# Optimization experiments

Hardware: AMD Instinct MI355X
Metric: run time of the kernel (lower is better)

## Reference

```python
import jax, jax.numpy as jnp
import numpy as np

B, S, D = 2, 2048, 2048
QH, KVH, HD = 32, 8, 64
GRP = QH // KVH  # GQA group size = 4


def setup_inputs() -> dict:
    key = jax.random.key(0)
    ks = jax.random.split(key, 9)
    x = jax.random.normal(ks[0], (B, S, D), jnp.float32)
    # RoPE angle table: [S, HD//2] -> stacked (cos, sin) -> [S, HD//2, 2]
    inv_freq = 1.0 / (10000.0 ** (np.arange(0, HD, 2, dtype=np.float32) / HD))
    ang = np.arange(S, dtype=np.float32)[:, None] * inv_freq[None, :]
    freqs = jnp.stack([jnp.cos(jnp.asarray(ang)), jnp.sin(jnp.asarray(ang))], axis=-1).astype(jnp.float32)
    w = 0.02
    Wq = jax.random.normal(ks[1], (D, QH * HD), jnp.float32) * w
    bq = jnp.zeros((QH * HD,), jnp.float32)
    Wk = jax.random.normal(ks[2], (D, KVH * HD), jnp.float32) * w
    bk = jnp.zeros((KVH * HD,), jnp.float32)
    Wv = jax.random.normal(ks[3], (D, KVH * HD), jnp.float32) * w
    bv = jnp.zeros((KVH * HD,), jnp.float32)
    Wo = jax.random.normal(ks[4], (QH * HD, D), jnp.float32) * w
    bo = jnp.zeros((D,), jnp.float32)
    return {"x": x, "freqs": freqs, "Wq": Wq, "bq": bq, "Wk": Wk, "bk": bk,
            "Wv": Wv, "bv": bv, "Wo": Wo, "bo": bo}


def _rope(xh, cos, sin):
    # xh: [b, s, h, hd]; complex rotation on adjacent pairs, like view_as_complex
    b, s, h, hd = xh.shape
    xp = xh.reshape(b, s, h, hd // 2, 2)
    x0, x1 = xp[..., 0], xp[..., 1]
    o0 = x0 * cos - x1 * sin
    o1 = x0 * sin + x1 * cos
    return jnp.stack([o0, o1], axis=-1).reshape(b, s, h, hd)


def reference(x, freqs, Wq, bq, Wk, bk, Wv, bv, Wo, bo):
    b, s, _ = x.shape
    q = (x @ Wq + bq).reshape(b, s, QH, HD)
    k = (x @ Wk + bk).reshape(b, s, KVH, HD)
    v = (x @ Wv + bv).reshape(b, s, KVH, HD)
    cos = freqs[:s, :, 0][None, :, None, :]  # [1, s, 1, hd//2]
    sin = freqs[:s, :, 1][None, :, None, :]
    q = _rope(q, cos, sin)
    k = _rope(k, cos, sin)
    # [b, h, s, hd]
    q = q.transpose(0, 2, 1, 3).reshape(b, KVH, GRP, s, HD)
    k = k.transpose(0, 2, 1, 3)  # [b, kvh, s, hd]
    v = v.transpose(0, 2, 1, 3)
    scores = jnp.einsum('bkgsh,bkth->bkgst', q, k) / jnp.sqrt(jnp.float32(HD))
    attn = jax.nn.softmax(scores, axis=-1)
    o = jnp.einsum('bkgst,bkth->bkgsh', attn, v)  # [b, kvh, grp, s, hd]
    o = o.reshape(b, QH, s, HD).transpose(0, 2, 1, 3).reshape(b, s, QH * HD)
    return o @ Wo + bo
```

## Files before the change

### kernel.cpp

```cpp
#include <hip/hip_runtime.h>
#include <stdint.h>

#define B_   2
#define S_   2048
#define D_   2048
#define QH_  32
#define KVH_ 8
#define HD_  64

typedef short  short8  __attribute__((ext_vector_type(8)));
typedef float  floatx4 __attribute__((ext_vector_type(4)));

__device__ __forceinline__ ushort f2b(float f) {
  union { float f; uint32_t u; } c; c.f = f;
  uint32_t u = c.u;
  return (ushort)((u + 0x7FFFu + ((u >> 16) & 1u)) >> 16);
}

__device__ __forceinline__ uint32_t fbits(float f) {
  union { float f; uint32_t u; } c; c.f = f;
  return c.u;
}

__device__ __forceinline__ short8 mk8(uint32_t a, uint32_t b, uint32_t c, uint32_t d) {
  union { uint4 u; short8 s; } v; v.u = (uint4){a, b, c, d}; return v.s;
}

__device__ __forceinline__ uint32_t cvtpk(float a, float b) {
  uint32_t r;
  asm("v_cvt_pk_bf16_f32 %0, %1, %2" : "=v"(r) : "v"(a), "v"(b));
  return r;
}

__device__ __forceinline__ void dma16(const void* g, void* l) {
  __builtin_amdgcn_global_load_lds(
      (const __attribute__((address_space(1))) uint32_t*)(uintptr_t)g,
      (__attribute__((address_space(3))) uint32_t*)(uintptr_t)l, 16, 0, 0);
}

#define QSCALE 0.18033688f


__global__ __launch_bounds__(256) void conv_x_kernel(const float* __restrict__ X,
                                                     ushort* __restrict__ Xb) {
  size_t i = ((size_t)blockIdx.x * 256 + threadIdx.x) * 4;
  float4 v = *(const float4*)(X + i);
  ushort4 o;
  o.x = f2b(v.x); o.y = f2b(v.y); o.z = f2b(v.z); o.w = f2b(v.w);
  *(ushort4*)(Xb + i) = o;
}

__global__ void tconv_all_kernel(const float* __restrict__ Wq, const float* __restrict__ Wk,
                                 const float* __restrict__ Wv, const float* __restrict__ Wo,
                                 ushort* __restrict__ wqkv, ushort* __restrict__ wo) {
  __shared__ float tile[32][33];
  int z = blockIdx.z;
  const float* W; ushort* Wt; int N;
  if (z == 0)      { W = Wq; Wt = wqkv;                        N = 2048; }
  else if (z == 1) { W = Wk; Wt = wqkv + (size_t)2048 * 2048;  N = 512;  }
  else if (z == 2) { W = Wv; Wt = wqkv + (size_t)2560 * 2048;  N = 512;  }
  else             { W = Wo; Wt = wo;                          N = 2048; }
  int bx = blockIdx.x, by = blockIdx.y;
  if (bx * 32 >= N) return;
  int tx = threadIdx.x, ty = threadIdx.y;
#pragma unroll
  for (int i = 0; i < 32; i += 8)
    tile[ty + i][tx] = W[(size_t)(by * 32 + ty + i) * N + bx * 32 + tx];
  __syncthreads();
#pragma unroll
  for (int i = 0; i < 32; i += 8)
    Wt[(size_t)(bx * 32 + ty + i) * 2048 + by * 32 + tx] = f2b(tile[tx][ty + i]);
}

__global__ void bias_kernel(const float* __restrict__ bq, const float* __restrict__ bk,
                            const float* __restrict__ bv, float* __restrict__ outb) {
  int i = blockIdx.x * 256 + threadIdx.x;
  if (i >= 3072) return;
  float v;
  if (i < 2048)      v = bq[i];
  else if (i < 2560) v = bk[i - 2048];
  else               v = bv[i - 2560];
  outb[i] = v;
}


__global__ __launch_bounds__(256) void gemm_qkv_kernel(
    const ushort* __restrict__ A, const ushort* __restrict__ Bt,
    const float* __restrict__ bias, const float2* __restrict__ F2,
    ushort* __restrict__ qb, ushort* __restrict__ kb, ushort* __restrict__ vb) {
  const int K = 2048;
  __shared__ ushort sA[2][128 * 32];
  __shared__ ushort sB[2][128 * 32];
  const int tid  = threadIdx.x;
  const int bm   = blockIdx.y, bn = blockIdx.x;
  const int wave = tid >> 6, lane = tid & 63;
  const int quad = lane >> 4, l16 = lane & 15;
  const int wm   = (wave >> 1) * 64, wn = (wave & 1) * 64;

  const ushort* Ab = A  + (size_t)(bm * 128) * K;
  const ushort* Bb = Bt + (size_t)(bn * 128) * K;

  const int gr = lane >> 2;
  const int gu = (lane & 3) * 8;

  floatx4 acc[4][4];
#pragma unroll
  for (int i = 0; i < 4; i++)
#pragma unroll
    for (int j = 0; j < 4; j++) acc[i][j] = (floatx4){0.f, 0.f, 0.f, 0.f};

#pragma unroll
  for (int j = 0; j < 2; j++) {
    int row = j * 64 + wave * 16 + gr;
    dma16(Ab + (size_t)row * K + gu, &sA[0][j * 2048 + wave * 512]);
    dma16(Bb + (size_t)row * K + gu, &sB[0][j * 2048 + wave * 512]);
  }

  int cur = 0;
  for (int k0 = 0; k0 < K; k0 += 32) {
    __syncthreads();
    if (k0 + 32 < K) {
      int nxt = cur ^ 1;
#pragma unroll
      for (int j = 0; j < 2; j++) {
        int row = j * 64 + wave * 16 + gr;
        dma16(Ab + (size_t)row * K + k0 + 32 + gu, &sA[nxt][j * 2048 + wave * 512]);
        dma16(Bb + (size_t)row * K + k0 + 32 + gu, &sB[nxt][j * 2048 + wave * 512]);
      }
    }
    short8 af[4], bf[4];
#pragma unroll
    for (int mi = 0; mi < 4; mi++)
      af[mi] = *(const short8*)&sA[cur][(wm + mi * 16 + l16) * 32 + quad * 8];
#pragma unroll
    for (int ni = 0; ni < 4; ni++)
      bf[ni] = *(const short8*)&sB[cur][(wn + ni * 16 + l16) * 32 + quad * 8];
#pragma unroll
    for (int mi = 0; mi < 4; mi++)
#pragma unroll
      for (int ni = 0; ni < 4; ni++)
        acc[mi][ni] = __builtin_amdgcn_mfma_f32_16x16x32_bf16(
            af[mi], bf[ni], acc[mi][ni], 0, 0, 0);
    cur ^= 1;
  }

  const int isQ = (bn < 16);
  const int isV = (bn >= 20);
  const int hh  = wn >> 6;
  const float sySign = (l16 & 1) ? 1.f : -1.f;
  ushort* dst;
  int hbase;
  if (isQ)      { dst = qb; hbase = bn * 2 + hh; }
  else if (!isV){ dst = kb; hbase = (bn - 16) * 2 + hh; }
  else          { dst = vb; hbase = (bn - 20) * 2 + hh; }
  const int NH = isQ ? QH_ : KVH_;

  float bvv[4];
#pragma unroll
  for (int ni = 0; ni < 4; ni++)
    bvv[ni] = bias[bn * 128 + wn + ni * 16 + l16];

#pragma unroll
  for (int mi = 0; mi < 4; mi++) {
#pragma unroll
    for (int r = 0; r < 4; r++) {
      int row = bm * 128 + wm + mi * 16 + quad * 4 + r;
      int s = row & 2047, bb = row >> 11;
      size_t base = (((size_t)bb * NH + hbase) * S_ + s) * HD_ + l16 * 4;
      ushort4 pk;
      if (!isV) {
        float o[4];
#pragma unroll
        for (int ni = 0; ni < 4; ni++) {
          float xv = acc[mi][ni][r] + bvv[ni];
          float2 cs = F2[s * 32 + ni * 8 + (l16 >> 1)];
          float pp = __shfl_xor(xv, 1);
          float oo = fmaf(pp * sySign, cs.y, xv * cs.x);
          if (isQ) oo *= QSCALE;
          o[ni] = oo;
        }
        pk.x = f2b(o[0]); pk.y = f2b(o[1]); pk.z = f2b(o[2]); pk.w = f2b(o[3]);
      } else {
        pk.x = f2b(acc[mi][0][r] + bvv[0]);
        pk.y = f2b(acc[mi][1][r] + bvv[1]);
        pk.z = f2b(acc[mi][2][r] + bvv[2]);
        pk.w = f2b(acc[mi][3][r] + bvv[3]);
      }
      *(ushort4*)&dst[base] = pk;
    }
  }
}


__global__ __launch_bounds__(256) void gemm_bt_kernel(
    const ushort* __restrict__ A, const ushort* __restrict__ Bt,
    const float* __restrict__ bias, float* __restrict__ C,
    int M, int N, int K) {
  __shared__ ushort sA[2][128 * 32];
  __shared__ ushort sB[2][128 * 32];
  const int tid  = threadIdx.x;
  const int bm   = blockIdx.y, bn = blockIdx.x;
  const int wave = tid >> 6, lane = tid & 63;
  const int quad = lane >> 4, l16 = lane & 15;
  const int wm   = (wave >> 1) * 64, wn = (wave & 1) * 64;

  const ushort* Ab = A  + (size_t)(bm * 128) * K;
  const ushort* Bb = Bt + (size_t)(bn * 128) * K;

  const int gr = lane >> 2;
  const int gu = (lane & 3) * 8;

  floatx4 acc[4][4];
#pragma unroll
  for (int i = 0; i < 4; i++)
#pragma unroll
    for (int j = 0; j < 4; j++) acc[i][j] = (floatx4){0.f, 0.f, 0.f, 0.f};

#pragma unroll
  for (int j = 0; j < 2; j++) {
    int row = j * 64 + wave * 16 + gr;
    dma16(Ab + (size_t)row * K + gu, &sA[0][j * 2048 + wave * 512]);
    dma16(Bb + (size_t)row * K + gu, &sB[0][j * 2048 + wave * 512]);
  }

  int cur = 0;
  for (int k0 = 0; k0 < K; k0 += 32) {
    __syncthreads();
    if (k0 + 32 < K) {
      int nxt = cur ^ 1;
#pragma unroll
      for (int j = 0; j < 2; j++) {
        int row = j * 64 + wave * 16 + gr;
        dma16(Ab + (size_t)row * K + k0 + 32 + gu, &sA[nxt][j * 2048 + wave * 512]);
        dma16(Bb + (size_t)row * K + k0 + 32 + gu, &sB[nxt][j * 2048 + wave * 512]);
      }
    }
    short8 af[4], bf[4];
#pragma unroll
    for (int mi = 0; mi < 4; mi++)
      af[mi] = *(const short8*)&sA[cur][(wm + mi * 16 + l16) * 32 + quad * 8];
#pragma unroll
    for (int ni = 0; ni < 4; ni++)
      bf[ni] = *(const short8*)&sB[cur][(wn + ni * 16 + l16) * 32 + quad * 8];
#pragma unroll
    for (int mi = 0; mi < 4; mi++)
#pragma unroll
      for (int ni = 0; ni < 4; ni++)
        acc[mi][ni] = __builtin_amdgcn_mfma_f32_16x16x32_bf16(
            af[mi], bf[ni], acc[mi][ni], 0, 0, 0);
    cur ^= 1;
  }

#pragma unroll
  for (int mi = 0; mi < 4; mi++) {
#pragma unroll
    for (int ni = 0; ni < 4; ni++) {
      int col  = bn * 128 + wn + ni * 16 + l16;
      float bv = bias[col];
#pragma unroll
      for (int r = 0; r < 4; r++) {
        int row = bm * 128 + wm + mi * 16 + quad * 4 + r;
        C[(size_t)row * N + col] = acc[mi][ni][r] + bv;
      }
    }
  }
}


__global__ void vpack_kernel(const ushort* __restrict__ vb, ushort* __restrict__ Vt) {
  __shared__ ushort tile[64][65];
  int s0 = blockIdx.x * 64;
  int bh = blockIdx.y;
  int tx = threadIdx.x, ty = threadIdx.y;
#pragma unroll
  for (int i = 0; i < 64; i += 8)
    tile[ty + i][tx] = vb[((size_t)bh * S_ + s0 + ty + i) * HD_ + tx];
  __syncthreads();
#pragma unroll
  for (int i = 0; i < 64; i += 8) {
    int dp = ty + i;
    int dt = (dp & 3) * 16 + (dp >> 2);
    Vt[((size_t)bh * HD_ + dt) * S_ + s0 + tx] = tile[tx][dp];
  }
}


__global__ __launch_bounds__(512, 4) void attn_kernel(
    const ushort* __restrict__ Q, const ushort* __restrict__ K,
    const ushort* __restrict__ Vt, ushort* __restrict__ O) {
  const int qt = blockIdx.x, qh = blockIdx.y, b = blockIdx.z;
  const int kvh = qh >> 2;
  const int tid = threadIdx.x;
  const int wave = tid >> 6, lane = tid & 63;
  const int quad = lane >> 4, l16 = lane & 15;

  __shared__ ushort kBuf[2][64 * 64];
  __shared__ ushort vBuf[2][64 * 64];

  const ushort* Qh = Q  + ((size_t)(b * QH_ + qh)) * S_ * HD_;
  const ushort* Kh = K  + ((size_t)(b * KVH_ + kvh)) * S_ * HD_;
  const ushort* Vh = Vt + ((size_t)(b * KVH_ + kvh)) * HD_ * S_;

  const int dr = lane >> 3;
  const int du = (lane & 7) ^ (dr & 7);
  const size_t kLaneOff = (size_t)(wave * 8 + dr) * 64 + du * 8;
  const size_t vLaneOff = (size_t)(wave * 8 + dr) * S_ + du * 8;
  const int swz = l16 & 7;

  const int q0 = qt * 256 + wave * 32;
  short8 aq[2][2];
#pragma unroll
  for (int m = 0; m < 2; m++)
#pragma unroll
    for (int s2 = 0; s2 < 2; s2++)
      aq[m][s2] = *(const short8*)(Qh + (size_t)(q0 + m * 16 + l16) * HD_ + s2 * 32 + quad * 8);

  floatx4 oacc[2][4];
#pragma unroll
  for (int m = 0; m < 2; m++)
#pragma unroll
    for (int t = 0; t < 4; t++) oacc[m][t] = (floatx4){0.f, 0.f, 0.f, 0.f};
  float ls[2] = {0.f, 0.f};

  dma16(Kh + kLaneOff, &kBuf[0][wave * 512]);
  dma16(Vh + vLaneOff, &vBuf[0][wave * 512]);

  int cur = 0;
  for (int kv0 = 0; kv0 < S_; kv0 += 64) {
    __syncthreads();
    if (kv0 + 64 < S_) {
      int nxt = cur ^ 1;
      dma16(Kh + (size_t)(kv0 + 64) * 64 + kLaneOff, &kBuf[nxt][wave * 512]);
      dma16(Vh + (size_t)(kv0 + 64) + vLaneOff,      &vBuf[nxt][wave * 512]);
    }

#pragma unroll
    for (int u = 0; u < 2; u++) {
      uint32_t pk[2][4];
#pragma unroll
      for (int cc = 0; cc < 2; cc++) {
        const int c = u * 2 + cc;
        short8 kf0 = *(const short8*)&kBuf[cur][(c * 16 + l16) * 64 + ((quad ^ swz) * 8)];
        short8 kf1 = *(const short8*)&kBuf[cur][(c * 16 + l16) * 64 + (((4 + quad) ^ swz) * 8)];
#pragma unroll
        for (int m = 0; m < 2; m++) {
          floatx4 sc = (floatx4){0.f, 0.f, 0.f, 0.f};
          __builtin_amdgcn_s_setprio(1);
          sc = __builtin_amdgcn_mfma_f32_16x16x32_bf16(kf0, aq[m][0], sc, 0, 0, 0);
          sc = __builtin_amdgcn_mfma_f32_16x16x32_bf16(kf1, aq[m][1], sc, 0, 0, 0);
          __builtin_amdgcn_s_setprio(0);
          float p0 = __builtin_amdgcn_exp2f(sc[0]);
          float p1 = __builtin_amdgcn_exp2f(sc[1]);
          float p2 = __builtin_amdgcn_exp2f(sc[2]);
          float p3 = __builtin_amdgcn_exp2f(sc[3]);
          ls[m] += (p0 + p1) + (p2 + p3);
          pk[m][cc * 2 + 0] = cvtpk(p0, p1);
          pk[m][cc * 2 + 1] = cvtpk(p2, p3);
        }
      }
#pragma unroll
      for (int t = 0; t < 4; t++) {
        const int row = (t * 16 + l16) * 64;
        uint2 v0 = *(const uint2*)&vBuf[cur][row + (((u * 4 + (quad >> 1)) ^ swz) * 8) + (quad & 1) * 4];
        uint2 v1 = *(const uint2*)&vBuf[cur][row + (((u * 4 + 2 + (quad >> 1)) ^ swz) * 8) + (quad & 1) * 4];
        short8 vf = mk8(v0.x, v0.y, v1.x, v1.y);
        __builtin_amdgcn_s_setprio(1);
#pragma unroll
        for (int m = 0; m < 2; m++) {
          short8 ap = mk8(pk[m][0], pk[m][1], pk[m][2], pk[m][3]);
          oacc[m][t] = __builtin_amdgcn_mfma_f32_16x16x32_bf16(ap, vf, oacc[m][t], 0, 0, 0);
        }
        __builtin_amdgcn_s_setprio(0);
      }
    }
    cur ^= 1;
  }

#pragma unroll
  for (int m = 0; m < 2; m++) {
    ls[m] += __shfl_xor(ls[m], 16);
    ls[m] += __shfl_xor(ls[m], 32);
  }
#pragma unroll
  for (int m = 0; m < 2; m++) {
#pragma unroll
    for (int r = 0; r < 4; r++) {
      float l = __shfl(ls[m], (lane & 48) | (quad * 4 + r));
      float inv = 1.0f / l;
      int srow = q0 + m * 16 + quad * 4 + r;
      size_t base = ((size_t)b * S_ + srow) * (QH_ * HD_) + (size_t)qh * HD_;
#pragma unroll
      for (int t = 0; t < 4; t++)
        O[base + t * 16 + l16] = f2b(oacc[m][t][r] * inv);
    }
  }
}


extern "C" void kernel_launch(void* const* d_in, const int* in_sizes, int n_in,
                              void* d_out, int out_size, void* d_ws, size_t ws_size,
                              hipStream_t stream) {
  const float* x  = (const float*)d_in[0];
  const float* fr = (const float*)d_in[1];
  const float* Wq = (const float*)d_in[2];
  const float* bq = (const float*)d_in[3];
  const float* Wk = (const float*)d_in[4];
  const float* bk = (const float*)d_in[5];
  const float* Wv = (const float*)d_in[6];
  const float* bv = (const float*)d_in[7];
  const float* Wo = (const float*)d_in[8];
  const float* bo = (const float*)d_in[9];
  float* out = (float*)d_out;
  char* ws = (char*)d_ws;

  ushort* xb    = (ushort*)(ws + 0);
  ushort* wqkv  = (ushort*)(ws + 16777216);
  ushort* wo    = (ushort*)(ws + 29360128);
  float*  biasq = (float* )(ws + 37748736);
  ushort* qb    = (ushort*)(ws + 37761024);
  ushort* kb    = (ushort*)(ws + 54538240);
  ushort* vb    = (ushort*)(ws + 58732544);
  ushort* vt    = (ushort*)(ws + 62926848);
  ushort* ob    = xb;

  conv_x_kernel<<<8192, 256, 0, stream>>>(x, xb);
  tconv_all_kernel<<<dim3(64, 64, 4), dim3(32, 8), 0, stream>>>(Wq, Wk, Wv, Wo, wqkv, wo);
  bias_kernel<<<12, 256, 0, stream>>>(bq, bk, bv, biasq);

  gemm_qkv_kernel<<<dim3(3072 / 128, 4096 / 128), 256, 0, stream>>>(
      xb, wqkv, biasq, (const float2*)fr, qb, kb, vb);

  vpack_kernel<<<dim3(2048 / 64, 16), dim3(64, 8), 0, stream>>>(vb, vt);

  attn_kernel<<<dim3(8, 32, 2), 512, 0, stream>>>(qb, kb, vt, ob);

  gemm_bt_kernel<<<dim3(2048 / 128, 4096 / 128), 256, 0, stream>>>(
      ob, wo, bo, out, 4096, 2048, 2048);
}
```

Before: 316.9 us.

## Merge prep kernels into one launch and halve attention rows per wave

Combines the x bf16 conversion, the weight transpose-convert and the bias concatenation into a single prep kernel launch, removing two launches. The attention kernel now gives each wave 16 query rows instead of 32 and doubles the grid to 16 q-tiles. It also raises the launch-bounds occupancy hint to 8. This gives more blocks and higher occupancy, at the cost of loading and streaming the K/V tiles twice as often per query row, which lowers data reuse.

```diff
diff --git a/kernel.cpp b/kernel.cpp
--- a/kernel.cpp
+++ b/kernel.cpp
@@ -41,20 +41,36 @@
 #define QSCALE 0.18033688f
 
 
-__global__ __launch_bounds__(256) void conv_x_kernel(const float* __restrict__ X,
-                                                     ushort* __restrict__ Xb) {
-  size_t i = ((size_t)blockIdx.x * 256 + threadIdx.x) * 4;
-  float4 v = *(const float4*)(X + i);
-  ushort4 o;
-  o.x = f2b(v.x); o.y = f2b(v.y); o.z = f2b(v.z); o.w = f2b(v.w);
-  *(ushort4*)(Xb + i) = o;
-}
-
-__global__ void tconv_all_kernel(const float* __restrict__ Wq, const float* __restrict__ Wk,
-                                 const float* __restrict__ Wv, const float* __restrict__ Wo,
-                                 ushort* __restrict__ wqkv, ushort* __restrict__ wo) {
+__global__ void prep_kernel(const float* __restrict__ Wq, const float* __restrict__ Wk,
+                            const float* __restrict__ Wv, const float* __restrict__ Wo,
+                            const float* __restrict__ X,  const float* __restrict__ bq,
+                            const float* __restrict__ bk, const float* __restrict__ bv,
+                            ushort* __restrict__ wqkv, ushort* __restrict__ wo,
+                            ushort* __restrict__ Xb, float* __restrict__ biasq) {
   __shared__ float tile[32][33];
   int z = blockIdx.z;
+  int tx = threadIdx.x, ty = threadIdx.y;
+  if (z == 4) {
+    int bid = blockIdx.y * 64 + blockIdx.x;
+    int tid = ty * 32 + tx;
+    size_t i = ((size_t)bid * 256 + tid) * 8;
+    float4 v0 = *(const float4*)(X + i);
+    float4 v1 = *(const float4*)(X + i + 4);
+    ushort4 o0, o1;
+    o0.x = f2b(v0.x); o0.y = f2b(v0.y); o0.z = f2b(v0.z); o0.w = f2b(v0.w);
+    o1.x = f2b(v1.x); o1.y = f2b(v1.y); o1.z = f2b(v1.z); o1.w = f2b(v1.w);
+    *(ushort4*)(Xb + i)     = o0;
+    *(ushort4*)(Xb + i + 4) = o1;
+    int gi = bid * 256 + tid;
+    if (gi < 3072) {
+      float v;
+      if (gi < 2048)      v = bq[gi];
+      else if (gi < 2560) v = bk[gi - 2048];
+      else                v = bv[gi - 2560];
+      biasq[gi] = v;
+    }
+    return;
+  }
   const float* W; ushort* Wt; int N;
   if (z == 0)      { W = Wq; Wt = wqkv;                        N = 2048; }
   else if (z == 1) { W = Wk; Wt = wqkv + (size_t)2048 * 2048;  N = 512;  }
@@ -62,7 +78,6 @@
   else             { W = Wo; Wt = wo;                          N = 2048; }
   int bx = blockIdx.x, by = blockIdx.y;
   if (bx * 32 >= N) return;
-  int tx = threadIdx.x, ty = threadIdx.y;
 #pragma unroll
   for (int i = 0; i < 32; i += 8)
     tile[ty + i][tx] = W[(size_t)(by * 32 + ty + i) * N + bx * 32 + tx];
@@ -70,17 +85,6 @@
 #pragma unroll
   for (int i = 0; i < 32; i += 8)
     Wt[(size_t)(bx * 32 + ty + i) * 2048 + by * 32 + tx] = f2b(tile[tx][ty + i]);
-}
-
-__global__ void bias_kernel(const float* __restrict__ bq, const float* __restrict__ bk,
-                            const float* __restrict__ bv, float* __restrict__ outb) {
-  int i = blockIdx.x * 256 + threadIdx.x;
-  if (i >= 3072) return;
-  float v;
-  if (i < 2048)      v = bq[i];
-  else if (i < 2560) v = bk[i - 2048];
-  else               v = bv[i - 2560];
-  outb[i] = v;
 }
 
 
@@ -285,7 +289,7 @@
 }
 
 
-__global__ __launch_bounds__(512, 4) void attn_kernel(
+__global__ __launch_bounds__(512, 8) void attn_kernel(
     const ushort* __restrict__ Q, const ushort* __restrict__ K,
     const ushort* __restrict__ Vt, ushort* __restrict__ O) {
   const int qt = blockIdx.x, qh = blockIdx.y, b = blockIdx.z;
@@ -307,20 +311,16 @@
   const size_t vLaneOff = (size_t)(wave * 8 + dr) * S_ + du * 8;
   const int swz = l16 & 7;
 
-  const int q0 = qt * 256 + wave * 32;
-  short8 aq[2][2];
-#pragma unroll
-  for (int m = 0; m < 2; m++)
-#pragma unroll
-    for (int s2 = 0; s2 < 2; s2++)
-      aq[m][s2] = *(const short8*)(Qh + (size_t)(q0 + m * 16 + l16) * HD_ + s2 * 32 + quad * 8);
-
-  floatx4 oacc[2][4];
-#pragma unroll
-  for (int m = 0; m < 2; m++)
-#pragma unroll
-    for (int t = 0; t < 4; t++) oacc[m][t] = (floatx4){0.f, 0.f, 0.f, 0.f};
-  float ls[2] = {0.f, 0.f};
+  const int q0 = qt * 128 + wave * 16;
+  short8 aq[2];
+#pragma unroll
+  for (int s2 = 0; s2 < 2; s2++)
+    aq[s2] = *(const short8*)(Qh + (size_t)(q0 + l16) * HD_ + s2 * 32 + quad * 8);
+
+  floatx4 oacc[4];
+#pragma unroll
+  for (int t = 0; t < 4; t++) oacc[t] = (floatx4){0.f, 0.f, 0.f, 0.f};
+  float ls = 0.f;
 
   dma16(Kh + kLaneOff, &kBuf[0][wave * 512]);
   dma16(Vh + vLaneOff, &vBuf[0][wave * 512]);
@@ -336,28 +336,26 @@
 
 #pragma unroll
     for (int u = 0; u < 2; u++) {
-      uint32_t pk[2][4];
+      uint32_t pk[4];
 #pragma unroll
       for (int cc = 0; cc < 2; cc++) {
         const int c = u * 2 + cc;
         short8 kf0 = *(const short8*)&kBuf[cur][(c * 16 + l16) * 64 + ((quad ^ swz) * 8)];
         short8 kf1 = *(const short8*)&kBuf[cur][(c * 16 + l16) * 64 + (((4 + quad) ^ swz) * 8)];
-#pragma unroll
-        for (int m = 0; m < 2; m++) {
-          floatx4 sc = (floatx4){0.f, 0.f, 0.f, 0.f};
-          __builtin_amdgcn_s_setprio(1);
-          sc = __builtin_amdgcn_mfma_f32_16x16x32_bf16(kf0, aq[m][0], sc, 0, 0, 0);
-          sc = __builtin_amdgcn_mfma_f32_16x16x32_bf16(kf1, aq[m][1], sc, 0, 0, 0);
-          __builtin_amdgcn_s_setprio(0);
-          float p0 = __builtin_amdgcn_exp2f(sc[0]);
-          float p1 = __builtin_amdgcn_exp2f(sc[1]);
-          float p2 = __builtin_amdgcn_exp2f(sc[2]);
-          float p3 = __builtin_amdgcn_exp2f(sc[3]);
-          ls[m] += (p0 + p1) + (p2 + p3);
-          pk[m][cc * 2 + 0] = cvtpk(p0, p1);
-          pk[m][cc * 2 + 1] = cvtpk(p2, p3);
-        }
-      }
+        floatx4 sc = (floatx4){0.f, 0.f, 0.f, 0.f};
+        __builtin_amdgcn_s_setprio(1);
+        sc = __builtin_amdgcn_mfma_f32_16x16x32_bf16(kf0, aq[0], sc, 0, 0, 0);
+        sc = __builtin_amdgcn_mfma_f32_16x16x32_bf16(kf1, aq[1], sc, 0, 0, 0);
+        __builtin_amdgcn_s_setprio(0);
+        float p0 = __builtin_amdgcn_exp2f(sc[0]);
+        float p1 = __builtin_amdgcn_exp2f(sc[1]);
+        float p2 = __builtin_amdgcn_exp2f(sc[2]);
+        float p3 = __builtin_amdgcn_exp2f(sc[3]);
+        ls += (p0 + p1) + (p2 + p3);
+        pk[cc * 2 + 0] = cvtpk(p0, p1);
+        pk[cc * 2 + 1] = cvtpk(p2, p3);
+      }
+      short8 ap = mk8(pk[0], pk[1], pk[2], pk[3]);
 #pragma unroll
       for (int t = 0; t < 4; t++) {
         const int row = (t * 16 + l16) * 64;
@@ -365,34 +363,24 @@
         uint2 v1 = *(const uint2*)&vBuf[cur][row + (((u * 4 + 2 + (quad >> 1)) ^ swz) * 8) + (quad & 1) * 4];
         short8 vf = mk8(v0.x, v0.y, v1.x, v1.y);
         __builtin_amdgcn_s_setprio(1);
-#pragma unroll
-        for (int m = 0; m < 2; m++) {
-          short8 ap = mk8(pk[m][0], pk[m][1], pk[m][2], pk[m][3]);
-          oacc[m][t] = __builtin_amdgcn_mfma_f32_16x16x32_bf16(ap, vf, oacc[m][t], 0, 0, 0);
-        }
+        oacc[t] = __builtin_amdgcn_mfma_f32_16x16x32_bf16(ap, vf, oacc[t], 0, 0, 0);
         __builtin_amdgcn_s_setprio(0);
       }
     }
     cur ^= 1;
   }
 
-#pragma unroll
-  for (int m = 0; m < 2; m++) {
-    ls[m] += __shfl_xor(ls[m], 16);
-    ls[m] += __shfl_xor(ls[m], 32);
-  }
-#pragma unroll
-  for (int m = 0; m < 2; m++) {
-#pragma unroll
-    for (int r = 0; r < 4; r++) {
-      float l = __shfl(ls[m], (lane & 48) | (quad * 4 + r));
-      float inv = 1.0f / l;
-      int srow = q0 + m * 16 + quad * 4 + r;
-      size_t base = ((size_t)b * S_ + srow) * (QH_ * HD_) + (size_t)qh * HD_;
-#pragma unroll
-      for (int t = 0; t < 4; t++)
-        O[base + t * 16 + l16] = f2b(oacc[m][t][r] * inv);
-    }
+  ls += __shfl_xor(ls, 16);
+  ls += __shfl_xor(ls, 32);
+#pragma unroll
+  for (int r = 0; r < 4; r++) {
+    float l = __shfl(ls, (lane & 48) | (quad * 4 + r));
+    float inv = 1.0f / l;
+    int srow = q0 + quad * 4 + r;
+    size_t base = ((size_t)b * S_ + srow) * (QH_ * HD_) + (size_t)qh * HD_;
+#pragma unroll
+    for (int t = 0; t < 4; t++)
+      O[base + t * 16 + l16] = f2b(oacc[t][r] * inv);
   }
 }
 
@@ -423,16 +411,15 @@
   ushort* vt    = (ushort*)(ws + 62926848);
   ushort* ob    = xb;
 
-  conv_x_kernel<<<8192, 256, 0, stream>>>(x, xb);
-  tconv_all_kernel<<<dim3(64, 64, 4), dim3(32, 8), 0, stream>>>(Wq, Wk, Wv, Wo, wqkv, wo);
-  bias_kernel<<<12, 256, 0, stream>>>(bq, bk, bv, biasq);
+  prep_kernel<<<dim3(64, 64, 5), dim3(32, 8), 0, stream>>>(
+      Wq, Wk, Wv, Wo, x, bq, bk, bv, wqkv, wo, xb, biasq);
 
   gemm_qkv_kernel<<<dim3(3072 / 128, 4096 / 128), 256, 0, stream>>>(
       xb, wqkv, biasq, (const float2*)fr, qb, kb, vb);
 
   vpack_kernel<<<dim3(2048 / 64, 16), dim3(64, 8), 0, stream>>>(vb, vt);
 
-  attn_kernel<<<dim3(8, 32, 2), 512, 0, stream>>>(qb, kb, vt, ob);
+  attn_kernel<<<dim3(16, 32, 2), 512, 0, stream>>>(qb, kb, vt, ob);
 
   gemm_bt_kernel<<<dim3(2048 / 128, 4096 / 128), 256, 0, stream>>>(
       ob, wo, bo, out, 4096, 2048, 2048);
```

Measured after the change: 330.4 us. 1.04x slower.
